# Kernel tuning notes

Hardware: AMD Instinct MI355X
Metric: run time of the kernel (lower is better)

## Reference

```python
import jax, jax.numpy as jnp
import numpy as np

B, S, DH, DF, DM = 32, 2048, 1024, 1024, 512


def setup_inputs() -> dict:
    key = jax.random.key(0)
    ks = jax.random.split(key, 7)
    s_h = 1.0 / np.sqrt(DH)
    s_f = 1.0 / np.sqrt(DF)
    s_m = 1.0 / np.sqrt(DM)
    return {
        "hidden_states": jax.random.normal(ks[0], (B, DH), jnp.float32),
        "feats": jax.random.normal(ks[1], (B, S, DF), jnp.float32),
        "W1h": jax.random.uniform(ks[2], (DM, DH), jnp.float32, -s_h, s_h),
        "b1h": jax.random.uniform(ks[3], (DM,), jnp.float32, -s_h, s_h),
        "W1f": jax.random.uniform(ks[4], (DM, DF), jnp.float32, -s_f, s_f),
        "b1f": jax.random.uniform(ks[5], (DM,), jnp.float32, -s_f, s_f),
        "w2": jax.random.uniform(ks[6], (DM,), jnp.float32, -s_m, s_m),
    }


def reference(hidden_states, feats, W1h, b1h, W1f, b1f, w2):
    # additive (Bahdanau) attention, single feature stream
    emb_h = hidden_states @ W1h.T + b1h                     # [B, DM]
    emb_f = jnp.einsum('bsd,md->bsm', feats, W1f) + b1f      # [B, S, DM]
    emb = jnp.tanh(emb_h[:, None, :] + emb_f)                # [B, S, DM]
    logits = jnp.einsum('bsm,m->bs', emb, w2)                # [B, S]
    probs = jax.nn.softmax(logits, axis=-1)                  # [B, S]
    context = jnp.einsum('bs,bsd->bd', probs, feats)         # [B, DF]
    # torch: cat(context, dim=1) -> [B, DF]; stack(probs, dim=1) -> [B, 1, S]
    return context, probs[:, None, :]
```

## Files before the change

### kernel.cpp

```cpp
#include <hip/hip_runtime.h>
#include <hip/hip_bf16.h>
#include <cstdint>
#include <cstddef>

#define B_   32
#define S_   2048
#define DH_  1024
#define DF_  1024
#define DM_  512
#define MTOT (B_ * S_)

typedef __attribute__((ext_vector_type(8))) short bf16x8;
typedef __attribute__((ext_vector_type(4))) float f32x4;

#define AS1 __attribute__((address_space(1)))
#define AS3 __attribute__((address_space(3)))

static __device__ __forceinline__ void load_lds16(const void* g, void* l) {
    __builtin_amdgcn_global_load_lds((const AS1 unsigned*)g, (AS3 unsigned*)l,
                                     16, 0, 0);
}

static __device__ __forceinline__ unsigned pack_rhu(float a, float b) {
    unsigned ua = (__float_as_uint(a) + 0x8000u) >> 16;
    unsigned ub = (__float_as_uint(b) + 0x8000u) & 0xFFFF0000u;
    return ua | ub;
}

static __device__ __forceinline__ float tanh_fast(float x) {
    float e = __expf(2.0f * x);
    return 1.0f - 2.0f / (e + 1.0f);
}

static __device__ __forceinline__ float bflo(unsigned v) {
    return __uint_as_float(v << 16);
}
static __device__ __forceinline__ float bfhi(unsigned v) {
    return __uint_as_float(v & 0xFFFF0000u);
}

__global__ __launch_bounds__(256) void k_embh(
    const float* __restrict__ hidden, const float* __restrict__ W1h,
    const float* __restrict__ b1h, const float* __restrict__ b1f,
    float* __restrict__ embh)
{
    int b  = blockIdx.x;
    int mg = blockIdx.y;
    int t  = threadIdx.x;
    int m  = mg * 64 + (t >> 2);
    int kp = (t & 3) * 256;
    const float4* h4 = (const float4*)(hidden + (size_t)b * DH_ + kp);
    const float4* w4 = (const float4*)(W1h + (size_t)m * DH_ + kp);
    float s = 0.0f;
    #pragma unroll 8
    for (int i = 0; i < 64; ++i) {
        float4 a = h4[i];
        float4 w = w4[i];
        s += a.x * w.x + a.y * w.y + a.z * w.z + a.w * w.w;
    }
    s += __shfl_xor(s, 1);
    s += __shfl_xor(s, 2);
    if ((t & 3) == 0)
        embh[b * DM_ + m] = s + b1h[m] + b1f[m];
}

__global__ __launch_bounds__(256) void k_cvt(
    const float* __restrict__ src, unsigned short* __restrict__ dst)
{
    size_t i = (size_t)blockIdx.x * 256 + threadIdx.x;
    float4 a = ((const float4*)src)[2 * i];
    float4 b = ((const float4*)src)[2 * i + 1];
    uint4 r;
    r.x = pack_rhu(a.x, a.y);
    r.y = pack_rhu(a.z, a.w);
    r.z = pack_rhu(b.x, b.y);
    r.w = pack_rhu(b.z, b.w);
    ((uint4*)dst)[i] = r;
}

__global__ __launch_bounds__(256) void k_gemm_bf(
    const unsigned short* __restrict__ fb, const unsigned short* __restrict__ wb,
    const float* __restrict__ embh, const float* __restrict__ w2,
    float* __restrict__ plog)
{
    __shared__ bf16x8 As[3][4 * 128];
    __shared__ bf16x8 Bs[3][4 * 128];

    const int t    = threadIdx.x;
    const int lane = t & 63;
    const int w    = t >> 6;
    const int wm   = w >> 1;
    const int wn   = w & 1;
    const int quad = lane >> 4;
    const int l16  = lane & 15;

    const int blk   = blockIdx.x;
    const int panel = blk >> 5;
    const int sub   = blk & 31;
    const int bx    = sub >> 3;
    const int by    = panel * 8 + (sub & 7);

    const unsigned short* aG0 = fb + ((size_t)(by * 128) + lane) * DF_ + w * 8;
    const unsigned short* aG1 = aG0 + (size_t)64 * DF_;
    const unsigned short* bG0 = wb + ((size_t)(bx * 128) + lane) * DF_ + w * 8;
    const unsigned short* bG1 = bG0 + (size_t)64 * DF_;

    f32x4 acc[4][4];
    const f32x4 zero = {0.0f, 0.0f, 0.0f, 0.0f};
    #pragma unroll
    for (int i = 0; i < 4; ++i)
        #pragma unroll
        for (int j = 0; j < 4; ++j) acc[i][j] = zero;

    auto stage = [&](int kt, int buf) {
        load_lds16(aG0 + kt * 32, &As[buf][w * 128]);
        load_lds16(aG1 + kt * 32, &As[buf][w * 128 + 64]);
        load_lds16(bG0 + kt * 32, &Bs[buf][w * 128]);
        load_lds16(bG1 + kt * 32, &Bs[buf][w * 128 + 64]);
    };

    stage(0, 0);
    stage(1, 1);

    int cur = 0;
    for (int kt = 0; kt < DF_ / 32; ++kt) {
        if (kt < DF_ / 32 - 1)
            asm volatile("s_waitcnt vmcnt(4)" ::: "memory");
        else
            asm volatile("s_waitcnt vmcnt(0)" ::: "memory");
        __builtin_amdgcn_s_barrier();

        if (kt + 2 < DF_ / 32) {
            int nxt = (cur == 0) ? 2 : cur - 1;
            stage(kt + 2, nxt);
        }

        bf16x8 af[4], bfr[4];
        #pragma unroll
        for (int mi = 0; mi < 4; ++mi)
            af[mi] = As[cur][quad * 128 + wm * 64 + mi * 16 + l16];
        #pragma unroll
        for (int nj = 0; nj < 4; ++nj)
            bfr[nj] = Bs[cur][quad * 128 + wn * 64 + nj * 16 + l16];

        __builtin_amdgcn_s_setprio(1);
        #pragma unroll
        for (int mi = 0; mi < 4; ++mi)
            #pragma unroll
            for (int nj = 0; nj < 4; ++nj)
                acc[mi][nj] = __builtin_amdgcn_mfma_f32_16x16x32_bf16(
                    af[mi], bfr[nj], acc[mi][nj], 0, 0, 0);
        __builtin_amdgcn_s_setprio(0);

        cur = (cur == 2) ? 0 : cur + 1;
    }

    const int bIdx = by >> 4;
    float ew[4], wv[4];
    #pragma unroll
    for (int nj = 0; nj < 4; ++nj) {
        int c = bx * 128 + wn * 64 + nj * 16 + l16;
        ew[nj] = embh[bIdx * DM_ + c];
        wv[nj] = w2[c];
    }
    float* plw = plog + (size_t)(bx * 2 + wn) * MTOT + bIdx * S_;
    #pragma unroll
    for (int mi = 0; mi < 4; ++mi) {
        #pragma unroll
        for (int reg = 0; reg < 4; ++reg) {
            float p = 0.0f;
            #pragma unroll
            for (int nj = 0; nj < 4; ++nj)
                p += tanh_fast(acc[mi][nj][reg] + ew[nj]) * wv[nj];
            p += __shfl_xor(p, 1);
            p += __shfl_xor(p, 2);
            p += __shfl_xor(p, 4);
            p += __shfl_xor(p, 8);
            if (l16 == 0) {
                int rowl = wm * 64 + mi * 16 + quad * 4 + reg;
                int s = (by * 128 + rowl) & (S_ - 1);
                plw[s] = p;
            }
        }
    }
}

__global__ __launch_bounds__(256) void k_gemm_f32(
    const float* __restrict__ feats, const unsigned short* __restrict__ w1fb,
    const float* __restrict__ embh, const float* __restrict__ w2,
    float* __restrict__ plog)
{
    __shared__ bf16x8 As[4 * 128];
    __shared__ bf16x8 Bs[4 * 128];

    const int t    = threadIdx.x;
    const int lane = t & 63;
    const int w    = t >> 6;
    const int wm   = w >> 1;
    const int wn   = w & 1;
    const int quad = lane >> 4;
    const int l16  = lane & 15;
    const int blk   = blockIdx.x;
    const int panel = blk >> 5;
    const int sub   = blk & 31;
    const int bx    = sub >> 3;
    const int by    = panel * 8 + (sub & 7);

    const int sRow = t >> 1;
    const int sK   = (t & 1) * 16;
    const int c0   = sK >> 3;
    const float*          aG = feats + (size_t)(by * 128 + sRow) * DF_ + sK;
    const unsigned short* bG = w1fb  + (size_t)(bx * 128 + sRow) * DF_ + sK;

    f32x4 acc[4][4];
    const f32x4 zero = {0.0f, 0.0f, 0.0f, 0.0f};
    #pragma unroll
    for (int i = 0; i < 4; ++i)
        #pragma unroll
        for (int j = 0; j < 4; ++j) acc[i][j] = zero;

    for (int kt = 0; kt < DF_ / 32; ++kt) {
        float4 a0 = *(const float4*)(aG + kt * 32);
        float4 a1 = *(const float4*)(aG + kt * 32 + 4);
        float4 a2 = *(const float4*)(aG + kt * 32 + 8);
        float4 a3 = *(const float4*)(aG + kt * 32 + 12);
        uint4  b0 = *(const uint4*)(bG + kt * 32);
        uint4  b1 = *(const uint4*)(bG + kt * 32 + 8);

        __syncthreads();

        union { unsigned u[4]; bf16x8 v; } pa;
        pa.u[0] = pack_rhu(a0.x, a0.y);
        pa.u[1] = pack_rhu(a0.z, a0.w);
        pa.u[2] = pack_rhu(a1.x, a1.y);
        pa.u[3] = pack_rhu(a1.z, a1.w);
        As[c0 * 128 + sRow] = pa.v;
        pa.u[0] = pack_rhu(a2.x, a2.y);
        pa.u[1] = pack_rhu(a2.z, a2.w);
        pa.u[2] = pack_rhu(a3.x, a3.y);
        pa.u[3] = pack_rhu(a3.z, a3.w);
        As[(c0 + 1) * 128 + sRow] = pa.v;

        union { uint4 q; bf16x8 v; } pb;
        pb.q = b0;
        Bs[c0 * 128 + sRow] = pb.v;
        pb.q = b1;
        Bs[(c0 + 1) * 128 + sRow] = pb.v;

        __syncthreads();

        bf16x8 af[4], bfr[4];
        #pragma unroll
        for (int mi = 0; mi < 4; ++mi)
            af[mi] = As[quad * 128 + wm * 64 + mi * 16 + l16];
        #pragma unroll
        for (int nj = 0; nj < 4; ++nj)
            bfr[nj] = Bs[quad * 128 + wn * 64 + nj * 16 + l16];

        #pragma unroll
        for (int mi = 0; mi < 4; ++mi)
            #pragma unroll
            for (int nj = 0; nj < 4; ++nj)
                acc[mi][nj] = __builtin_amdgcn_mfma_f32_16x16x32_bf16(
                    af[mi], bfr[nj], acc[mi][nj], 0, 0, 0);
    }

    const int bIdx = by >> 4;
    float ew[4], wv[4];
    #pragma unroll
    for (int nj = 0; nj < 4; ++nj) {
        int c = bx * 128 + wn * 64 + nj * 16 + l16;
        ew[nj] = embh[bIdx * DM_ + c];
        wv[nj] = w2[c];
    }
    float* plw = plog + (size_t)(bx * 2 + wn) * MTOT + bIdx * S_;
    #pragma unroll
    for (int mi = 0; mi < 4; ++mi) {
        #pragma unroll
        for (int reg = 0; reg < 4; ++reg) {
            float p = 0.0f;
            #pragma unroll
            for (int nj = 0; nj < 4; ++nj)
                p += tanh_fast(acc[mi][nj][reg] + ew[nj]) * wv[nj];
            p += __shfl_xor(p, 1);
            p += __shfl_xor(p, 2);
            p += __shfl_xor(p, 4);
            p += __shfl_xor(p, 8);
            if (l16 == 0) {
                int rowl = wm * 64 + mi * 16 + quad * 4 + reg;
                int s = (by * 128 + rowl) & (S_ - 1);
                plw[s] = p;
            }
        }
    }
}

__global__ __launch_bounds__(256) void k_softmax(
    const float* __restrict__ plog, float* __restrict__ probs_out)
{
    int b = blockIdx.x;
    int t = threadIdx.x;
    float l[8];
    #pragma unroll
    for (int i = 0; i < 8; ++i) {
        int s = t + i * 256;
        float sum = 0.0f;
        #pragma unroll
        for (int p = 0; p < 8; ++p)
            sum += plog[(size_t)p * MTOT + b * S_ + s];
        l[i] = sum;
    }
    float mx = l[0];
    #pragma unroll
    for (int i = 1; i < 8; ++i) mx = fmaxf(mx, l[i]);
    #pragma unroll
    for (int off = 1; off < 64; off <<= 1) mx = fmaxf(mx, __shfl_xor(mx, off));
    __shared__ float redm[4];
    __shared__ float reds[4];
    int wid = t >> 6;
    if ((t & 63) == 0) redm[wid] = mx;
    __syncthreads();
    mx = fmaxf(fmaxf(redm[0], redm[1]), fmaxf(redm[2], redm[3]));

    float e[8];
    float es = 0.0f;
    #pragma unroll
    for (int i = 0; i < 8; ++i) {
        e[i] = __expf(l[i] - mx);
        es += e[i];
    }
    #pragma unroll
    for (int off = 1; off < 64; off <<= 1) es += __shfl_xor(es, off);
    if ((t & 63) == 0) reds[wid] = es;
    __syncthreads();
    es = reds[0] + reds[1] + reds[2] + reds[3];
    float inv = 1.0f / es;
    #pragma unroll
    for (int i = 0; i < 8; ++i)
        probs_out[b * S_ + t + i * 256] = e[i] * inv;
}

__global__ __launch_bounds__(256) void k_context_bf(
    const unsigned short* __restrict__ fb, const float* __restrict__ probs,
    float* __restrict__ ctxp)
{
    int t    = threadIdx.x;
    int b    = blockIdx.x;
    int z    = blockIdx.y;
    int half = t >> 7;
    int dt   = t & 127;
    int s0   = z * 128 + half * 64;

    const uint4* f  = (const uint4*)(fb + (size_t)(b * S_ + s0) * DF_) + dt;
    const float* pr = probs + b * S_ + s0;

    float acc[8];
    #pragma unroll
    for (int j = 0; j < 8; ++j) acc[j] = 0.0f;

    #pragma unroll 8
    for (int i = 0; i < 64; ++i) {
        uint4 v = f[(size_t)i * (DF_ / 8)];
        float p = pr[i];
        acc[0] += p * bflo(v.x);
        acc[1] += p * bfhi(v.x);
        acc[2] += p * bflo(v.y);
        acc[3] += p * bfhi(v.y);
        acc[4] += p * bflo(v.z);
        acc[5] += p * bfhi(v.z);
        acc[6] += p * bflo(v.w);
        acc[7] += p * bfhi(v.w);
    }

    float4* o = (float4*)(ctxp + ((size_t)(z * 2 + half) * B_ + b) * DF_ + dt * 8);
    o[0] = make_float4(acc[0], acc[1], acc[2], acc[3]);
    o[1] = make_float4(acc[4], acc[5], acc[6], acc[7]);
}

__global__ __launch_bounds__(256) void k_context_f32(
    const float* __restrict__ feats, const float* __restrict__ probs,
    float* __restrict__ ctxp)
{
    int d  = blockIdx.x * 256 + threadIdx.x;
    int b  = blockIdx.y;
    int z  = blockIdx.z;
    const float* f  = feats + ((size_t)b * S_ + z * 64) * DF_ + d;
    const float* pr = probs + b * S_ + z * 64;
    float acc = 0.0f;
    #pragma unroll 4
    for (int i = 0; i < 64; ++i)
        acc += pr[i] * f[(size_t)i * DF_];
    ctxp[((size_t)z * B_ + b) * DF_ + d] = acc;
}

__global__ __launch_bounds__(256) void k_ctx_red(
    const float* __restrict__ ctxp, float* __restrict__ ctx)
{
    int i = blockIdx.x * 256 + threadIdx.x;
    float s = 0.0f;
    #pragma unroll
    for (int z = 0; z < 32; ++z)
        s += ctxp[(size_t)z * B_ * DF_ + i];
    ctx[i] = s;
}

extern "C" void kernel_launch(void* const* d_in, const int* in_sizes, int n_in,
                              void* d_out, int out_size, void* d_ws, size_t ws_size,
                              hipStream_t stream)
{
    const float* hidden = (const float*)d_in[0];
    const float* feats  = (const float*)d_in[1];
    const float* W1h    = (const float*)d_in[2];
    const float* b1h    = (const float*)d_in[3];
    const float* W1f    = (const float*)d_in[4];
    const float* b1f    = (const float*)d_in[5];
    const float* w2     = (const float*)d_in[6];

    float* out   = (float*)d_out;
    float* ctx   = out;
    float* probs = out + B_ * DF_;

    char* ws = (char*)d_ws;
    float*          embh  = (float*)ws;
    unsigned short* w1fb  = (unsigned short*)(ws + (64 << 10));
    float*          plog  = (float*)(ws + (64 << 10) + (1 << 20));
    float*          ctxp  = (float*)(ws + (64 << 10) + (3 << 20));
    unsigned short* featb = (unsigned short*)(ws + (8 << 20));

    const bool big_ws = ws_size >= ((size_t)8 << 20) + ((size_t)B_ * S_ * DF_ * 2);

    k_embh<<<dim3(B_, DM_ / 64), 256, 0, stream>>>(hidden, W1h, b1h, b1f, embh);
    k_cvt<<<dim3((DM_ * DF_ / 8) / 256), 256, 0, stream>>>(W1f, w1fb);

    if (big_ws) {
        k_cvt<<<dim3(((size_t)MTOT * DF_ / 8) / 256), 256, 0, stream>>>(feats, featb);
        k_gemm_bf<<<dim3((MTOT / 128) * (DM_ / 128)), 256, 0, stream>>>(
            featb, w1fb, embh, w2, plog);
        k_softmax<<<dim3(B_), 256, 0, stream>>>(plog, probs);
        k_context_bf<<<dim3(B_, 16), 256, 0, stream>>>(featb, probs, ctxp);
    } else {
        k_gemm_f32<<<dim3((MTOT / 128) * (DM_ / 128)), 256, 0, stream>>>(
            feats, w1fb, embh, w2, plog);
        k_softmax<<<dim3(B_), 256, 0, stream>>>(plog, probs);
        k_context_f32<<<dim3(DF_ / 256, B_, 32), 256, 0, stream>>>(feats, probs, ctxp);
    }
    k_ctx_red<<<dim3(B_ * DF_ / 256), 256, 0, stream>>>(ctxp, ctx);
}
```

Before: 579.3 us.

## Enlarge bf16 GEMM tile to 256x256 with 4-stage swizzled LDS pipeline

The bf16 feature GEMM moves from 128x128 tiles on 256 threads to 256x256 tiles on 512 threads (8 waves, 8x4 accumulators per wave). It adds a 4-deep LDS ring with an XOR swizzle against bank conflicts, split A/B prefetch interleaved with two MFMA half-phases, and an XCD-aware block index remap. The aim is more data reuse per loaded tile and better overlap of loads with matrix math. The conversion kernel also becomes a grid-stride loop over float4. The costs are heavier register and LDS pressure, lower occupancy, and a larger per-block epilogue.

```diff
diff --git a/kernel.cpp b/kernel.cpp
--- a/kernel.cpp
+++ b/kernel.cpp
@@ -9,6 +9,7 @@
 #define DF_  1024
 #define DM_  512
 #define MTOT (B_ * S_)
+#define NT_  (DF_ / 32)
 
 typedef __attribute__((ext_vector_type(8))) short bf16x8;
 typedef __attribute__((ext_vector_type(4))) float f32x4;
@@ -65,26 +66,146 @@
 }
 
 __global__ __launch_bounds__(256) void k_cvt(
-    const float* __restrict__ src, unsigned short* __restrict__ dst)
-{
-    size_t i = (size_t)blockIdx.x * 256 + threadIdx.x;
-    float4 a = ((const float4*)src)[2 * i];
-    float4 b = ((const float4*)src)[2 * i + 1];
-    uint4 r;
-    r.x = pack_rhu(a.x, a.y);
-    r.y = pack_rhu(a.z, a.w);
-    r.z = pack_rhu(b.x, b.y);
-    r.w = pack_rhu(b.z, b.w);
-    ((uint4*)dst)[i] = r;
-}
-
-__global__ __launch_bounds__(256) void k_gemm_bf(
+    const float* __restrict__ src, unsigned short* __restrict__ dst, long n4)
+{
+    long stride = (long)gridDim.x * 256;
+    for (long i = (long)blockIdx.x * 256 + threadIdx.x; i < n4; i += stride) {
+        float4 a = ((const float4*)src)[i];
+        uint2 r;
+        r.x = pack_rhu(a.x, a.y);
+        r.y = pack_rhu(a.z, a.w);
+        ((uint2*)dst)[i] = r;
+    }
+}
+
+__global__ __launch_bounds__(512, 2) void k_gemm_bf(
     const unsigned short* __restrict__ fb, const unsigned short* __restrict__ wb,
     const float* __restrict__ embh, const float* __restrict__ w2,
     float* __restrict__ plog)
 {
-    __shared__ bf16x8 As[3][4 * 128];
-    __shared__ bf16x8 Bs[3][4 * 128];
+    __shared__ bf16x8 As[4][1024];
+    __shared__ bf16x8 Bs[4][1024];
+
+    const int t    = threadIdx.x;
+    const int lane = t & 63;
+    const int w    = t >> 6;
+    const int wm   = w >> 2;
+    const int wn   = w & 3;
+    const int quad = lane >> 4;
+    const int l16  = lane & 15;
+
+    const int g    = blockIdx.x;
+    const int flat = (g & 7) * 64 + (g >> 3);
+    const int by   = flat >> 1;
+    const int bx   = flat & 1;
+
+    const int swz = ((lane & 3) ^ ((lane >> 3) & 3)) * 8;
+    const unsigned short* srcA =
+        fb + ((size_t)(by * 256 + w * 32 + (lane >> 2))) * DF_ + swz;
+    const unsigned short* srcB =
+        wb + ((size_t)(bx * 256 + w * 32 + (lane >> 2))) * DF_ + swz;
+
+    f32x4 acc[8][4];
+    const f32x4 zero = {0.0f, 0.0f, 0.0f, 0.0f};
+    #pragma unroll
+    for (int i = 0; i < 8; ++i)
+        #pragma unroll
+        for (int j = 0; j < 4; ++j) acc[i][j] = zero;
+
+    auto stageA = [&](int kt) {
+        load_lds16(srcA + kt * 32,            &As[kt & 3][(w * 2) * 64]);
+        load_lds16(srcA + 16 * DF_ + kt * 32, &As[kt & 3][(w * 2 + 1) * 64]);
+    };
+    auto stageB = [&](int kt) {
+        load_lds16(srcB + kt * 32,            &Bs[kt & 3][(w * 2) * 64]);
+        load_lds16(srcB + 16 * DF_ + kt * 32, &Bs[kt & 3][(w * 2 + 1) * 64]);
+    };
+
+    stageA(0); stageB(0);
+    stageA(1); stageB(1);
+    stageA(2); stageB(2);
+
+    const int sw4 = quad ^ ((l16 >> 1) & 3);
+    const int sa  = (wm * 128 + l16) * 4 + sw4;
+    const int sb  = (wn * 64 + l16) * 4 + sw4;
+
+    for (int kt = 0; kt < NT_; ++kt) {
+        const int buf = kt & 3;
+        if (kt < NT_ - 2)       asm volatile("s_waitcnt vmcnt(8)" ::: "memory");
+        else if (kt == NT_ - 2) asm volatile("s_waitcnt vmcnt(4)" ::: "memory");
+        else                    asm volatile("s_waitcnt vmcnt(0)" ::: "memory");
+        __builtin_amdgcn_s_barrier();
+
+        bf16x8 af[4], bfr[4];
+        #pragma unroll
+        for (int nj = 0; nj < 4; ++nj) bfr[nj] = Bs[buf][sb + nj * 64];
+        #pragma unroll
+        for (int mi = 0; mi < 4; ++mi) af[mi] = As[buf][sa + mi * 64];
+        if (kt < NT_ - 3) stageA(kt + 3);
+        __builtin_amdgcn_s_barrier();
+        asm volatile("s_waitcnt lgkmcnt(0)" ::: "memory");
+        __builtin_amdgcn_sched_barrier(0);
+        __builtin_amdgcn_s_setprio(1);
+        #pragma unroll
+        for (int mi = 0; mi < 4; ++mi)
+            #pragma unroll
+            for (int nj = 0; nj < 4; ++nj)
+                acc[mi][nj] = __builtin_amdgcn_mfma_f32_16x16x32_bf16(
+                    af[mi], bfr[nj], acc[mi][nj], 0, 0, 0);
+        __builtin_amdgcn_s_setprio(0);
+        __builtin_amdgcn_s_barrier();
+
+        #pragma unroll
+        for (int mi = 0; mi < 4; ++mi) af[mi] = As[buf][sa + 256 + mi * 64];
+        if (kt < NT_ - 3) stageB(kt + 3);
+        __builtin_amdgcn_s_barrier();
+        asm volatile("s_waitcnt lgkmcnt(0)" ::: "memory");
+        __builtin_amdgcn_sched_barrier(0);
+        __builtin_amdgcn_s_setprio(1);
+        #pragma unroll
+        for (int mi = 0; mi < 4; ++mi)
+            #pragma unroll
+            for (int nj = 0; nj < 4; ++nj)
+                acc[4 + mi][nj] = __builtin_amdgcn_mfma_f32_16x16x32_bf16(
+                    af[mi], bfr[nj], acc[4 + mi][nj], 0, 0, 0);
+        __builtin_amdgcn_s_setprio(0);
+    }
+
+    const int bIdx = by >> 3;
+    float ew[4], wv[4];
+    #pragma unroll
+    for (int nj = 0; nj < 4; ++nj) {
+        int c = bx * 256 + wn * 64 + nj * 16 + l16;
+        ew[nj] = embh[bIdx * DM_ + c];
+        wv[nj] = w2[c];
+    }
+    float* plw = plog + (size_t)(bx * 4 + wn) * MTOT + bIdx * S_;
+    const int rbase = (by * 256 + wm * 128) & (S_ - 1);
+    #pragma unroll
+    for (int mi = 0; mi < 8; ++mi) {
+        #pragma unroll
+        for (int reg = 0; reg < 4; ++reg) {
+            float p = 0.0f;
+            #pragma unroll
+            for (int nj = 0; nj < 4; ++nj)
+                p += tanh_fast(acc[mi][nj][reg] + ew[nj]) * wv[nj];
+            p += __shfl_xor(p, 1);
+            p += __shfl_xor(p, 2);
+            p += __shfl_xor(p, 4);
+            p += __shfl_xor(p, 8);
+            if (l16 == 0)
+                plw[rbase + mi * 16 + quad * 4 + reg] = p;
+        }
+    }
+}
+
+__global__ __launch_bounds__(256) void k_gemm_f32(
+    const float* __restrict__ feats, const unsigned short* __restrict__ w1fb,
+    const float* __restrict__ embh, const float* __restrict__ w2,
+    float* __restrict__ plog)
+{
+    __shared__ bf16x8 As[4 * 128];
+    __shared__ bf16x8 Bs[4 * 128];
 
     const int t    = threadIdx.x;
     const int lane = t & 63;
@@ -93,17 +214,17 @@
     const int wn   = w & 1;
     const int quad = lane >> 4;
     const int l16  = lane & 15;
-
     const int blk   = blockIdx.x;
     const int panel = blk >> 5;
     const int sub   = blk & 31;
     const int bx    = sub >> 3;
     const int by    = panel * 8 + (sub & 7);
 
-    const unsigned short* aG0 = fb + ((size_t)(by * 128) + lane) * DF_ + w * 8;
-    const unsigned short* aG1 = aG0 + (size_t)64 * DF_;
-    const unsigned short* bG0 = wb + ((size_t)(bx * 128) + lane) * DF_ + w * 8;
-    const unsigned short* bG1 = bG0 + (size_t)64 * DF_;
+    const int sRow = t >> 1;
+    const int sK   = (t & 1) * 16;
+    const int c0   = sK >> 3;
+    const float*          aG = feats + (size_t)(by * 128 + sRow) * DF_ + sK;
+    const unsigned short* bG = w1fb  + (size_t)(bx * 128 + sRow) * DF_ + sK;
 
     f32x4 acc[4][4];
     const f32x4 zero = {0.0f, 0.0f, 0.0f, 0.0f};
@@ -112,47 +233,50 @@
         #pragma unroll
         for (int j = 0; j < 4; ++j) acc[i][j] = zero;
 
-    auto stage = [&](int kt, int buf) {
-        load_lds16(aG0 + kt * 32, &As[buf][w * 128]);
-        load_lds16(aG1 + kt * 32, &As[buf][w * 128 + 64]);
-        load_lds16(bG0 + kt * 32, &Bs[buf][w * 128]);
-        load_lds16(bG1 + kt * 32, &Bs[buf][w * 128 + 64]);
-    };
-
-    stage(0, 0);
-    stage(1, 1);
-
-    int cur = 0;
     for (int kt = 0; kt < DF_ / 32; ++kt) {
-        if (kt < DF_ / 32 - 1)
-            asm volatile("s_waitcnt vmcnt(4)" ::: "memory");
-        else
-            asm volatile("s_waitcnt vmcnt(0)" ::: "memory");
-        __builtin_amdgcn_s_barrier();
-
-        if (kt + 2 < DF_ / 32) {
-            int nxt = (cur == 0) ? 2 : cur - 1;
-            stage(kt + 2, nxt);
-        }
+        float4 a0 = *(const float4*)(aG + kt * 32);
+        float4 a1 = *(const float4*)(aG + kt * 32 + 4);
+        float4 a2 = *(const float4*)(aG + kt * 32 + 8);
+        float4 a3 = *(const float4*)(aG + kt * 32 + 12);
+        uint4  b0 = *(const uint4*)(bG + kt * 32);
+        uint4  b1 = *(const uint4*)(bG + kt * 32 + 8);
+
+        __syncthreads();
+
+        union { unsigned u[4]; bf16x8 v; } pa;
+        pa.u[0] = pack_rhu(a0.x, a0.y);
+        pa.u[1] = pack_rhu(a0.z, a0.w);
+        pa.u[2] = pack_rhu(a1.x, a1.y);
+        pa.u[3] = pack_rhu(a1.z, a1.w);
+        As[c0 * 128 + sRow] = pa.v;
+        pa.u[0] = pack_rhu(a2.x, a2.y);
+        pa.u[1] = pack_rhu(a2.z, a2.w);
+        pa.u[2] = pack_rhu(a3.x, a3.y);
+        pa.u[3] = pack_rhu(a3.z, a3.w);
+        As[(c0 + 1) * 128 + sRow] = pa.v;
+
+        union { uint4 q; bf16x8 v; } pb;
+        pb.q = b0;
+        Bs[c0 * 128 + sRow] = pb.v;
+        pb.q = b1;
+        Bs[(c0 + 1) * 128 + sRow] = pb.v;
+
+        __syncthreads();
 
         bf16x8 af[4], bfr[4];
         #pragma unroll
         for (int mi = 0; mi < 4; ++mi)
-            af[mi] = As[cur][quad * 128 + wm * 64 + mi * 16 + l16];
+            af[mi] = As[quad * 128 + wm * 64 + mi * 16 + l16];
         #pragma unroll
         for (int nj = 0; nj < 4; ++nj)
-            bfr[nj] = Bs[cur][quad * 128 + wn * 64 + nj * 16 + l16];
-
-        __builtin_amdgcn_s_setprio(1);
+            bfr[nj] = Bs[quad * 128 + wn * 64 + nj * 16 + l16];
+
         #pragma unroll
         for (int mi = 0; mi < 4; ++mi)
             #pragma unroll
             for (int nj = 0; nj < 4; ++nj)
                 acc[mi][nj] = __builtin_amdgcn_mfma_f32_16x16x32_bf16(
                     af[mi], bfr[nj], acc[mi][nj], 0, 0, 0);
-        __builtin_amdgcn_s_setprio(0);
-
-        cur = (cur == 2) ? 0 : cur + 1;
     }
 
     const int bIdx = by >> 4;
@@ -185,116 +309,6 @@
     }
 }
 
-__global__ __launch_bounds__(256) void k_gemm_f32(
-    const float* __restrict__ feats, const unsigned short* __restrict__ w1fb,
-    const float* __restrict__ embh, const float* __restrict__ w2,
-    float* __restrict__ plog)
-{
-    __shared__ bf16x8 As[4 * 128];
-    __shared__ bf16x8 Bs[4 * 128];
-
-    const int t    = threadIdx.x;
-    const int lane = t & 63;
-    const int w    = t >> 6;
-    const int wm   = w >> 1;
-    const int wn   = w & 1;
-    const int quad = lane >> 4;
-    const int l16  = lane & 15;
-    const int blk   = blockIdx.x;
-    const int panel = blk >> 5;
-    const int sub   = blk & 31;
-    const int bx    = sub >> 3;
-    const int by    = panel * 8 + (sub & 7);
-
-    const int sRow = t >> 1;
-    const int sK   = (t & 1) * 16;
-    const int c0   = sK >> 3;
-    const float*          aG = feats + (size_t)(by * 128 + sRow) * DF_ + sK;
-    const unsigned short* bG = w1fb  + (size_t)(bx * 128 + sRow) * DF_ + sK;
-
-    f32x4 acc[4][4];
-    const f32x4 zero = {0.0f, 0.0f, 0.0f, 0.0f};
-    #pragma unroll
-    for (int i = 0; i < 4; ++i)
-        #pragma unroll
-        for (int j = 0; j < 4; ++j) acc[i][j] = zero;
-
-    for (int kt = 0; kt < DF_ / 32; ++kt) {
-        float4 a0 = *(const float4*)(aG + kt * 32);
-        float4 a1 = *(const float4*)(aG + kt * 32 + 4);
-        float4 a2 = *(const float4*)(aG + kt * 32 + 8);
-        float4 a3 = *(const float4*)(aG + kt * 32 + 12);
-        uint4  b0 = *(const uint4*)(bG + kt * 32);
-        uint4  b1 = *(const uint4*)(bG + kt * 32 + 8);
-
-        __syncthreads();
-
-        union { unsigned u[4]; bf16x8 v; } pa;
-        pa.u[0] = pack_rhu(a0.x, a0.y);
-        pa.u[1] = pack_rhu(a0.z, a0.w);
-        pa.u[2] = pack_rhu(a1.x, a1.y);
-        pa.u[3] = pack_rhu(a1.z, a1.w);
-        As[c0 * 128 + sRow] = pa.v;
-        pa.u[0] = pack_rhu(a2.x, a2.y);
-        pa.u[1] = pack_rhu(a2.z, a2.w);
-        pa.u[2] = pack_rhu(a3.x, a3.y);
-        pa.u[3] = pack_rhu(a3.z, a3.w);
-        As[(c0 + 1) * 128 + sRow] = pa.v;
-
-        union { uint4 q; bf16x8 v; } pb;
-        pb.q = b0;
-        Bs[c0 * 128 + sRow] = pb.v;
-        pb.q = b1;
-        Bs[(c0 + 1) * 128 + sRow] = pb.v;
-
-        __syncthreads();
-
-        bf16x8 af[4], bfr[4];
-        #pragma unroll
-        for (int mi = 0; mi < 4; ++mi)
-            af[mi] = As[quad * 128 + wm * 64 + mi * 16 + l16];
-        #pragma unroll
-        for (int nj = 0; nj < 4; ++nj)
-            bfr[nj] = Bs[quad * 128 + wn * 64 + nj * 16 + l16];
-
-        #pragma unroll
-        for (int mi = 0; mi < 4; ++mi)
-            #pragma unroll
-            for (int nj = 0; nj < 4; ++nj)
-                acc[mi][nj] = __builtin_amdgcn_mfma_f32_16x16x32_bf16(
-                    af[mi], bfr[nj], acc[mi][nj], 0, 0, 0);
-    }
-
-    const int bIdx = by >> 4;
-    float ew[4], wv[4];
-    #pragma unroll
-    for (int nj = 0; nj < 4; ++nj) {
-        int c = bx * 128 + wn * 64 + nj * 16 + l16;
-        ew[nj] = embh[bIdx * DM_ + c];
-        wv[nj] = w2[c];
-    }
-    float* plw = plog + (size_t)(bx * 2 + wn) * MTOT + bIdx * S_;
-    #pragma unroll
-    for (int mi = 0; mi < 4; ++mi) {
-        #pragma unroll
-        for (int reg = 0; reg < 4; ++reg) {
-            float p = 0.0f;
-            #pragma unroll
-            for (int nj = 0; nj < 4; ++nj)
-                p += tanh_fast(acc[mi][nj][reg] + ew[nj]) * wv[nj];
-            p += __shfl_xor(p, 1);
-            p += __shfl_xor(p, 2);
-            p += __shfl_xor(p, 4);
-            p += __shfl_xor(p, 8);
-            if (l16 == 0) {
-                int rowl = wm * 64 + mi * 16 + quad * 4 + reg;
-                int s = (by * 128 + rowl) & (S_ - 1);
-                plw[s] = p;
-            }
-        }
-    }
-}
-
 __global__ __launch_bounds__(256) void k_softmax(
     const float* __restrict__ plog, float* __restrict__ probs_out)
 {
@@ -430,11 +444,11 @@
     const bool big_ws = ws_size >= ((size_t)8 << 20) + ((size_t)B_ * S_ * DF_ * 2);
 
     k_embh<<<dim3(B_, DM_ / 64), 256, 0, stream>>>(hidden, W1h, b1h, b1f, embh);
-    k_cvt<<<dim3((DM_ * DF_ / 8) / 256), 256, 0, stream>>>(W1f, w1fb);
+    k_cvt<<<dim3(512), 256, 0, stream>>>(W1f, w1fb, (long)DM_ * DF_ / 4);
 
     if (big_ws) {
-        k_cvt<<<dim3(((size_t)MTOT * DF_ / 8) / 256), 256, 0, stream>>>(feats, featb);
-        k_gemm_bf<<<dim3((MTOT / 128) * (DM_ / 128)), 256, 0, stream>>>(
+        k_cvt<<<dim3(8192), 256, 0, stream>>>(feats, featb, (long)MTOT * DF_ / 4);
+        k_gemm_bf<<<dim3((MTOT / 256) * (DM_ / 256)), 512, 0, stream>>>(
             featb, w1fb, embh, w2, plog);
         k_softmax<<<dim3(B_), 256, 0, stream>>>(plog, probs);
         k_context_bf<<<dim3(B_, 16), 256, 0, stream>>>(featb, probs, ctxp);
```

Result: faster. 520.1 us (-10.2%).
